# Optimization experiments

Measured on AMD Instinct MI355X. Metric: run time of the kernel, lower is better.

## Reference

```python
import jax, jax.numpy as jnp
import numpy as np

NODE_DIM = 2
EMB_DIM = 128
SEQ_LEN = 5000
BATCH = 64


def _cyclic_positional_encoding(n_position, emb_dim, mean_pooling=True):
    """Faithful numpy port of EmbeddingNet.Cyclic_Positional_Encoding (init-time constant)."""
    Td_set = np.linspace(np.power(n_position, 1 / (emb_dim // 2)), n_position, emb_dim // 2, dtype='int')
    x = np.zeros((n_position, emb_dim))
    for i in range(emb_dim):
        Td = Td_set[i // 3 * 3 + 1] if i // 3 * 3 + 1 < emb_dim // 2 else Td_set[-1]
        fai = 0 if i <= emb_dim // 2 else 2 * np.pi * ((-i + emb_dim // 2) / (emb_dim // 2))
        longer = np.arange(0, np.ceil(n_position / Td) * Td, 0.01)
        idx = np.linspace(0, len(longer), n_position, dtype='int', endpoint=False)
        base = 2 * np.pi / Td * np.abs(np.mod(longer, 2 * Td) - Td) + fai
        x[:, i] = (np.cos(base) if i % 2 == 1 else np.sin(base))[idx]
    pat = x.astype(np.float32)
    ar = np.arange(n_position)
    shifts = [-2, -1, 0, 1, 2] if mean_pooling else [0]
    acc = np.zeros_like(pat)
    for s in shifts:
        acc += pat[(ar + s + n_position) % n_position]
    pat = acc / float(len(shifts)) - pat.mean(0)
    return jnp.asarray(pat, dtype=jnp.float32)


def setup_inputs() -> dict:
    key = jax.random.key(0)
    kx, kw, ks = jax.random.split(key, 3)
    x = jax.random.normal(kx, (BATCH, SEQ_LEN, NODE_DIM), dtype=jnp.float32)
    stdv = 1.0 / np.sqrt(NODE_DIM)
    W = jax.random.uniform(kw, (EMB_DIM, NODE_DIM), dtype=jnp.float32, minval=-stdv, maxval=stdv)
    pattern = _cyclic_positional_encoding(SEQ_LEN, EMB_DIM)  # [S, D]

    # solutions must be a single-cycle successor permutation over SEQ_LEN nodes
    def make_cycle(k):
        p = jax.random.permutation(k, SEQ_LEN)
        return jnp.zeros(SEQ_LEN, jnp.int32).at[p].set(jnp.roll(p, -1).astype(jnp.int32))

    solutions = jax.vmap(make_cycle)(jax.random.split(ks, BATCH))  # [B, S] int32
    return {"x": x, "W": W, "pattern": pattern, "solutions": solutions}


def reference(x, W, pattern, solutions):
    B, S = solutions.shape
    # pointer-chase: pre=0; visited_time[solutions[pre]] = i+1; pre = solutions[pre]
    def step(pre, _):
        nxt = jnp.take_along_axis(solutions, pre[:, None], axis=1)[:, 0]
        return nxt, nxt

    _, order = jax.lax.scan(step, jnp.zeros(B, dtype=solutions.dtype), None, length=S)
    order = order.T  # [B, S]: node visited at step i
    visited_time = jnp.zeros((B, S), jnp.int32).at[
        jnp.arange(B)[:, None], order
    ].set(jnp.arange(1, S + 1, dtype=jnp.int32)[None, :])
    idx = visited_time % S  # [B, S]
    PFEs = pattern[idx]  # gather -> [B, S, D]
    NFEs = jnp.einsum('bsn,dn->bsd', x, W)  # Linear(node_dim->emb, no bias)
    return NFEs, PFEs, visited_time
```

## Files before the change

### kernel.cpp

```cpp
#include <hip/hip_runtime.h>

#define SEQ 5000
#define BATCH 64
#define DIM 128
#define PB 16
#define TPB 512

__global__ __launch_bounds__(TPB) void fused_kernel(
    const float2* __restrict__ x,
    const float4* __restrict__ W,
    const float4* __restrict__ pat,
    const int* __restrict__ sol,
    float* __restrict__ out) {
    __shared__ unsigned buf[2][SEQ];
    const int b  = blockIdx.x / PB;
    const int bi = blockIdx.x % PB;

    const int* sp = sol + b * SEQ;
    for (int i = threadIdx.x; i < SEQ; i += TPB) {
        unsigned nx = (unsigned)sp[i];
        if (nx >= SEQ) nx = 0;
        buf[0][i] = (i == 0) ? 0u : ((1u << 16) | nx);
    }
    __syncthreads();
    int cur = 0;
#pragma unroll 1
    for (int it = 0; it < 13; ++it) {
        for (int i = threadIdx.x; i < SEQ; i += TPB) {
            unsigned w  = buf[cur][i];
            unsigned w2 = buf[cur][w & 0xFFFFu];
            buf[cur ^ 1][i] = (w & 0xFFFF0000u) + w2;
        }
        __syncthreads();
        cur ^= 1;
    }

    const size_t NFE = (size_t)BATCH * SEQ * DIM;
    float4* nfe4 = (float4*)out;
    float4* pfe4 = (float4*)(out + NFE);
    float*  vt_out = out + 2 * NFE;

    const int c = threadIdx.x & 31;
    float4 wa = W[c * 2 + 0];
    float4 wb = W[c * 2 + 1];

    const int lo = (bi * SEQ) / PB, hi = ((bi + 1) * SEQ) / PB;
    for (int s = lo + (threadIdx.x >> 5); s < hi; s += TPB / 32) {
        unsigned dist = buf[cur][s] >> 16;
        int vt = SEQ - (int)dist;
        int i = (dist == 0u) ? 0 : vt;
        if ((unsigned)i >= SEQ) i = 0;
        const size_t r = (size_t)b * SEQ + s;

        float2 xv = x[r];
        float4 nv;
        nv.x = fmaf(xv.x, wa.x, xv.y * wa.y);
        nv.y = fmaf(xv.x, wa.z, xv.y * wa.w);
        nv.z = fmaf(xv.x, wb.x, xv.y * wb.y);
        nv.w = fmaf(xv.x, wb.z, xv.y * wb.w);
        nfe4[r * 32 + c] = nv;

        pfe4[r * 32 + c] = pat[(size_t)i * 32 + c];

        if (c == 0) vt_out[r] = (float)vt;
    }
}

extern "C" void kernel_launch(void* const* d_in, const int* in_sizes, int n_in,
                              void* d_out, int out_size, void* d_ws, size_t ws_size,
                              hipStream_t stream) {
    const void* xp = d_in[0];
    const void* wp = d_in[1];
    const void* pp = d_in[2];
    const void* sp = d_in[3];
    {
        const void* big[2] = {nullptr, nullptr};
        int nbig = 0;
        const void *w_ = nullptr, *s_ = nullptr;
        for (int i = 0; i < n_in; ++i) {
            if (in_sizes[i] == DIM * 2) w_ = d_in[i];
            else if (in_sizes[i] == BATCH * SEQ) s_ = d_in[i];
            else if (in_sizes[i] == SEQ * DIM && nbig < 2) big[nbig++] = d_in[i];
        }
        if (w_ && s_ && nbig == 2) { wp = w_; sp = s_; xp = big[0]; pp = big[1]; }
    }

    fused_kernel<<<BATCH * PB, TPB, 0, stream>>>(
        (const float2*)xp, (const float4*)wp, (const float4*)pp,
        (const int*)sp, (float*)d_out);
}
```

Measured before the change: 373.2 us.

## Split rank computation into its own kernel and stream emission separately

Moves the pointer-jumping list-ranking into a dedicated kernel that runs once per batch row instead of redundantly in each of sixteen blocks per row. A second grid-stride kernel reads the visited times back and writes the NFE and PFE outputs using nontemporal stores. This removes duplicated shared-memory ranking work. The cost is an extra launch, a round trip of the visited-time array through global memory, and a rank phase that uses only one block per batch row.

```diff
diff --git a/kernel.cpp b/kernel.cpp
--- a/kernel.cpp
+++ b/kernel.cpp
@@ -3,21 +3,22 @@
 #define SEQ 5000
 #define BATCH 64
 #define DIM 128
-#define PB 16
-#define TPB 512
 
-__global__ __launch_bounds__(TPB) void fused_kernel(
-    const float2* __restrict__ x,
-    const float4* __restrict__ W,
-    const float4* __restrict__ pat,
+#define TPB1 1024
+#define TPB2 512
+#define ROWS_PER_ITER (TPB2 / 32)
+#define EMIT_BLOCKS 2048
+
+typedef float f32x4 __attribute__((ext_vector_type(4)));
+
+__global__ __launch_bounds__(TPB1) void rank_kernel(
     const int* __restrict__ sol,
-    float* __restrict__ out) {
+    float* __restrict__ vt_out) {
     __shared__ unsigned buf[2][SEQ];
-    const int b  = blockIdx.x / PB;
-    const int bi = blockIdx.x % PB;
+    const int b = blockIdx.x;
+    const int* sp = sol + b * SEQ;
 
-    const int* sp = sol + b * SEQ;
-    for (int i = threadIdx.x; i < SEQ; i += TPB) {
+    for (int i = threadIdx.x; i < SEQ; i += TPB1) {
         unsigned nx = (unsigned)sp[i];
         if (nx >= SEQ) nx = 0;
         buf[0][i] = (i == 0) ? 0u : ((1u << 16) | nx);
@@ -26,7 +27,7 @@
     int cur = 0;
 #pragma unroll 1
     for (int it = 0; it < 13; ++it) {
-        for (int i = threadIdx.x; i < SEQ; i += TPB) {
+        for (int i = threadIdx.x; i < SEQ; i += TPB1) {
             unsigned w  = buf[cur][i];
             unsigned w2 = buf[cur][w & 0xFFFFu];
             buf[cur ^ 1][i] = (w & 0xFFFF0000u) + w2;
@@ -34,35 +35,43 @@
         __syncthreads();
         cur ^= 1;
     }
+    for (int i = threadIdx.x; i < SEQ; i += TPB1) {
+        int vt = SEQ - (int)(buf[cur][i] >> 16);
+        vt_out[(size_t)b * SEQ + i] = (float)vt;
+    }
+}
 
+__global__ __launch_bounds__(TPB2) void emit_kernel(
+    const float2* __restrict__ x,
+    const f32x4* __restrict__ W,
+    const f32x4* __restrict__ pat,
+    const float* __restrict__ vt_in,
+    float* __restrict__ out) {
     const size_t NFE = (size_t)BATCH * SEQ * DIM;
-    float4* nfe4 = (float4*)out;
-    float4* pfe4 = (float4*)(out + NFE);
-    float*  vt_out = out + 2 * NFE;
+    f32x4* nfe4 = (f32x4*)out;
+    f32x4* pfe4 = (f32x4*)(out + NFE);
 
     const int c = threadIdx.x & 31;
-    float4 wa = W[c * 2 + 0];
-    float4 wb = W[c * 2 + 1];
+    f32x4 wa = W[c * 2 + 0];
+    f32x4 wb = W[c * 2 + 1];
 
-    const int lo = (bi * SEQ) / PB, hi = ((bi + 1) * SEQ) / PB;
-    for (int s = lo + (threadIdx.x >> 5); s < hi; s += TPB / 32) {
-        unsigned dist = buf[cur][s] >> 16;
-        int vt = SEQ - (int)dist;
-        int i = (dist == 0u) ? 0 : vt;
+    const size_t TOT = (size_t)BATCH * SEQ;
+    for (size_t r = (size_t)blockIdx.x * ROWS_PER_ITER + (threadIdx.x >> 5);
+         r < TOT; r += (size_t)gridDim.x * ROWS_PER_ITER) {
+        int vt = (int)vt_in[r];
+        int i = (vt >= SEQ) ? 0 : vt;
         if ((unsigned)i >= SEQ) i = 0;
-        const size_t r = (size_t)b * SEQ + s;
 
         float2 xv = x[r];
-        float4 nv;
+        f32x4 nv;
         nv.x = fmaf(xv.x, wa.x, xv.y * wa.y);
         nv.y = fmaf(xv.x, wa.z, xv.y * wa.w);
         nv.z = fmaf(xv.x, wb.x, xv.y * wb.y);
         nv.w = fmaf(xv.x, wb.z, xv.y * wb.w);
-        nfe4[r * 32 + c] = nv;
+        __builtin_nontemporal_store(nv, &nfe4[r * 32 + c]);
 
-        pfe4[r * 32 + c] = pat[(size_t)i * 32 + c];
-
-        if (c == 0) vt_out[r] = (float)vt;
+        f32x4 pv = pat[(size_t)i * 32 + c];
+        __builtin_nontemporal_store(pv, &pfe4[r * 32 + c]);
     }
 }
 
@@ -85,7 +94,11 @@
         if (w_ && s_ && nbig == 2) { wp = w_; sp = s_; xp = big[0]; pp = big[1]; }
     }
 
-    fused_kernel<<<BATCH * PB, TPB, 0, stream>>>(
-        (const float2*)xp, (const float4*)wp, (const float4*)pp,
-        (const int*)sp, (float*)d_out);
+    const size_t NFE = (size_t)BATCH * SEQ * DIM;
+    float* vt_out = (float*)d_out + 2 * NFE;
+
+    rank_kernel<<<BATCH, TPB1, 0, stream>>>((const int*)sp, vt_out);
+    emit_kernel<<<EMIT_BLOCKS, TPB2, 0, stream>>>(
+        (const float2*)xp, (const f32x4*)wp, (const f32x4*)pp,
+        (const float*)vt_out, (float*)d_out);
 }
```

Result: faster. 351.5 us (-5.8%).
